# Kernel optimization log

Measured on AMD Instinct MI355X. Metric: run time of the kernel, lower is better.

## Reference

```python
import jax, jax.numpy as jnp
import numpy as np

N_FFT = 2048
HOP = 441
DIM = 512


def _hann(n_fft):
    # torch.hann_window (periodic): 0.5*(1 - cos(2*pi*n/N))
    n = jnp.arange(n_fft, dtype=jnp.float32)
    return 0.5 * (1.0 - jnp.cos(2.0 * jnp.pi * n / n_fft))


def setup_inputs() -> dict:
    key = jax.random.key(0)
    k1, k2, k3 = jax.random.split(key, 3)
    x = jax.random.normal(k1, (4, 2, 1323000), dtype=jnp.float32)
    W_enc = 1e-4 * jax.random.normal(k2, (DIM, N_FFT), dtype=jnp.float32)
    W_dec = 1e-4 * jax.random.normal(k3, (N_FFT, DIM), dtype=jnp.float32)
    return {"x": x, "W_enc": W_enc, "W_dec": W_dec, "length": 1323000}


def reference(x, W_enc, W_dec, length):
    b, c, L = x.shape
    pad = N_FFT // 2
    window = _hann(N_FFT)

    # ---- encode ----
    xp = jnp.pad(x, ((0, 0), (0, 0), (pad, pad)), mode="reflect")  # (b,c,L+n_fft)
    Lp = xp.shape[-1]
    t = (Lp - N_FFT) // HOP + 1  # num frames
    idx = jnp.arange(t)[:, None] * HOP + jnp.arange(N_FFT)[None, :]  # (t, n)
    frames = xp[..., idx] * window  # (b,c,t,n) -- the overlapping unfold buffer
    feat = jnp.einsum("bctn,mn->bctm", frames, W_enc)  # (b,c,t,dim)

    # ---- decode ----
    rec = jnp.einsum("bctm,nm->bctn", feat, W_dec)  # (b,c,t,n)
    L2 = N_FFT + (t - 1) * HOP
    # overlap-add (F.fold) over merged (b*c) rows
    out = jnp.zeros((b * c, L2), dtype=rec.dtype)
    out = out.at[:, idx].add(rec.reshape(b * c, t, N_FFT))
    # window normalization (second fold in the original)
    win_norm = jnp.zeros((L2,), dtype=rec.dtype)
    win_norm = win_norm.at[idx].add(jnp.broadcast_to(window, (t, N_FFT)))
    out = out / jnp.clip(win_norm, 1e-8)
    out = out.reshape(b, c, L2)[..., pad:pad + length]
    return out
```

## Files before the change

### kernel.cpp

```cpp
#include <hip/hip_runtime.h>
#include <stdint.h>

typedef unsigned short u16;
typedef unsigned int u32;
typedef __attribute__((ext_vector_type(8))) short short8;
typedef __attribute__((ext_vector_type(4))) float f32x4;

#define L_IN   1323000
#define PAD    1024
#define HOP    441
#define T_FR   3001
#define M_ROWS 24008
#define NB     3008
#define RPAD   448
#define K1E    2240
#define K2     2560
#define W_2PI_N 3.0679615757712823e-3f

__device__ __forceinline__ u16 f2bf(float f) {
  union { float f; u32 u; } v; v.f = f;
  u32 r = v.u + 0x7FFFu + ((v.u >> 16) & 1u);
  return (u16)(r >> 16);
}

__device__ __forceinline__ void gload16(const void* g, void* l) {
  __builtin_amdgcn_global_load_lds(
      (const __attribute__((address_space(1))) u32*)g,
      (__attribute__((address_space(3))) u32*)l, 16, 0, 0);
}

__global__ void prep_all(const float* __restrict__ x,
                         const float* __restrict__ W_enc, const float* __restrict__ W_dec,
                         u16* __restrict__ xb, u16* __restrict__ wh2,
                         u16* __restrict__ b2, float* __restrict__ zeros) {
  int stride = gridDim.x * blockDim.x;
  int tid0 = blockIdx.x * blockDim.x + threadIdx.x;
  for (int idx = tid0; idx < 64; idx += stride) zeros[idx] = 0.f;
  for (int idx = tid0; idx < 8 * NB * RPAD; idx += stride) {
    int bc = idx / (NB * RPAD);
    int rem = idx - bc * (NB * RPAD);
    int u = rem / RPAD;
    int r = rem - u * RPAD;
    int s = HOP * u + r - PAD;
    int ja = s < 0 ? -s : s;
    int jb = 2 * L_IN - 2 - ja;
    int jr = ja < jb ? ja : jb;
    xb[idx] = f2bf(x[(size_t)bc * L_IN + jr]);
  }
  for (int idx = tid0; idx < 512 * K1E; idx += stride) {
    int m = idx / K1E;
    int k = idx - m * K1E;
    int j = k / RPAD;
    int r = k - j * RPAD;
    int n = HOP * j + r;
    float v = 0.f;
    if (r < HOP && n < 2048)
      v = (0.5f - 0.5f * cosf(W_2PI_N * (float)n)) * W_enc[m * 2048 + n];
    wh2[idx] = f2bf(v);
  }
  for (int idx = tid0; idx < 512 * K2; idx += stride) {
    int r = idx / K2;
    int k = idx - r * K2;
    int j = k >> 9;
    int m = k & 511;
    int n = HOP * j + r;
    float v = (r < HOP && n < 2048) ? W_dec[n * 512 + m] : 0.f;
    b2[idx] = f2bf(v);
  }
}

__device__ __forceinline__ void mfma_tile(const u16* sA, const u16* sB, f32x4 acc[4][4],
                                          int lane, int wr, int wc) {
  const int lr = lane & 15;
  const int hi = lane >> 4;
  #pragma unroll
  for (int ks = 0; ks < 2; ++ks) {
    const int off = (((ks * 4 + hi) ^ (lr & 7)) << 3);
    short8 af[4], bg[4];
    #pragma unroll
    for (int f = 0; f < 4; ++f)
      af[f] = *(const short8*)(sA + (wr + f * 16 + lr) * 64 + off);
    #pragma unroll
    for (int f = 0; f < 4; ++f)
      bg[f] = *(const short8*)(sB + (wc + f * 16 + lr) * 64 + off);
    #pragma unroll
    for (int mf = 0; mf < 4; ++mf)
      #pragma unroll
      for (int nf = 0; nf < 4; ++nf)
        acc[mf][nf] = __builtin_amdgcn_mfma_f32_16x16x32_bf16(af[mf], bg[nf], acc[mf][nf], 0, 0, 0);
  }
}


__global__ __launch_bounds__(256, 2)
void gemm_enc(const u16* __restrict__ xb, const u16* __restrict__ wh2,
              u16* __restrict__ featb) {
  __shared__ u16 sA[128 * 64];
  __shared__ u16 sB[128 * 64];
  const int tid = threadIdx.x;
  const int lane = tid & 63;
  const int w = tid >> 6;
  const int m0 = blockIdx.x * 128;
  const int n0 = blockIdx.y * 128;
  const int colsw = (((lane & 7) ^ ((lane >> 3) & 7)) << 3);

  const u16* bsrc[4];
  const u16* asrc[4];
  #pragma unroll
  for (int i = 0; i < 4; ++i) {
    int row = (i * 4 + w) * 8 + (lane >> 3);
    bsrc[i] = wh2 + (size_t)(n0 + row) * K1E + colsw;
    int rg = m0 + row;
    int rgc = rg < M_ROWS ? rg : (M_ROWS - 1);
    int bc = rgc / T_FR;
    int t  = rgc - bc * T_FR;
    asrc[i] = xb + ((size_t)bc * NB + t) * RPAD + colsw;
  }

  f32x4 acc[4][4];
  #pragma unroll
  for (int a = 0; a < 4; ++a)
    #pragma unroll
    for (int b = 0; b < 4; ++b) acc[a][b] = f32x4{0.f, 0.f, 0.f, 0.f};

  const int wr = (w >> 1) * 64, wc = (w & 1) * 64;

  for (int kc = 0; kc < K1E; kc += 64) {
    __syncthreads();
    #pragma unroll
    for (int i = 0; i < 4; ++i)
      gload16(bsrc[i] + kc, &sB[(i * 4 + w) * 512]);
    #pragma unroll
    for (int i = 0; i < 4; ++i)
      gload16(asrc[i] + kc, &sA[(i * 4 + w) * 512]);
    __syncthreads();
    mfma_tile(sA, sB, acc, lane, wr, wc);
  }

  #pragma unroll
  for (int mf = 0; mf < 4; ++mf) {
    #pragma unroll
    for (int e = 0; e < 4; ++e) {
      int rg = m0 + wr + mf * 16 + ((lane >> 4) << 2) + e;
      if (rg < M_ROWS) {
        #pragma unroll
        for (int nf = 0; nf < 4; ++nf) {
          int cg = n0 + wc + nf * 16 + (lane & 15);
          featb[(size_t)rg * 512 + cg] = f2bf(acc[mf][nf][e]);
        }
      }
    }
  }
}


__global__ __launch_bounds__(256, 2)
void gemm_dec(const u16* __restrict__ featb, const u16* __restrict__ b2,
              const u16* __restrict__ zeros, float* __restrict__ out) {
  __shared__ u16 sA[128 * 64];
  __shared__ u16 sB[128 * 64];
  const int tid = threadIdx.x;
  const int lane = tid & 63;
  const int w = tid >> 6;
  const int m0 = blockIdx.x * 128;
  const int n0 = blockIdx.y * 128;
  const int colsw = (((lane & 7) ^ ((lane >> 3) & 7)) << 3);

  const u16* bsrc[4];
  const u16* fsrc[4];
  int qiv[4];
  unsigned vmask = 0;
  #pragma unroll
  for (int i = 0; i < 4; ++i) {
    int row = (i * 4 + w) * 8 + (lane >> 3);
    bsrc[i] = b2 + (size_t)(n0 + row) * K2 + colsw;
    int rg = m0 + row;
    int rgc = rg < M_ROWS ? rg : (M_ROWS - 1);
    int bc = rgc / T_FR;
    int qi = rgc - bc * T_FR;
    if (rg < M_ROWS) vmask |= 1u << i;
    qiv[i] = qi;
    fsrc[i] = featb + (size_t)(bc * T_FR + qi + 2) * 512 + colsw;
  }

  f32x4 acc[4][4];
  #pragma unroll
  for (int a = 0; a < 4; ++a)
    #pragma unroll
    for (int b = 0; b < 4; ++b) acc[a][b] = f32x4{0.f, 0.f, 0.f, 0.f};

  const int wr = (w >> 1) * 64, wc = (w & 1) * 64;

  for (int kc = 0; kc < K2; kc += 64) {
    int j = kc >> 9;
    __syncthreads();
    #pragma unroll
    for (int i = 0; i < 4; ++i)
      gload16(bsrc[i] + kc, &sB[(i * 4 + w) * 512]);
    #pragma unroll
    for (int i = 0; i < 4; ++i) {
      int t = qiv[i] + 2 - j;
      bool ok = ((vmask >> i) & 1) && (t >= 0) && (t <= 3000);
      const u16* pa = ok ? (fsrc[i] + kc - 1024 * j) : (zeros + colsw);
      gload16(pa, &sA[(i * 4 + w) * 512]);
    }
    __syncthreads();
    mfma_tile(sA, sB, acc, lane, wr, wc);
  }

  const int lr16 = lane & 15;
  float hh[4][5];
  float rnfull[4];
  int cgv[4];
  #pragma unroll
  for (int nf = 0; nf < 4; ++nf) {
    int cg = n0 + wc + nf * 16 + lr16;
    cgv[nf] = cg;
    float s = 0.f;
    #pragma unroll
    for (int j = 0; j < 5; ++j) {
      int n = HOP * j + cg;
      float h = (cg < HOP && n < 2048) ? (0.5f - 0.5f * cosf(W_2PI_N * (float)n)) : 0.f;
      hh[nf][j] = h;
      s += h;
    }
    rnfull[nf] = 1.f / fmaxf(s, 1e-8f);
  }

  #pragma unroll
  for (int mf = 0; mf < 4; ++mf) {
    #pragma unroll
    for (int e = 0; e < 4; ++e) {
      int rg = m0 + wr + mf * 16 + ((lane >> 4) << 2) + e;
      if (rg < M_ROWS) {
        int bc = rg / T_FR;
        int qi = rg - bc * T_FR;
        int ib = HOP * qi - 142;
        bool interior = (qi >= 2) && (qi <= 2998);
        #pragma unroll
        for (int nf = 0; nf < 4; ++nf) {
          if (cgv[nf] < HOP) {
            int oi = ib + cgv[nf];
            if (oi >= 0 && oi < L_IN) {
              float rn;
              if (interior) {
                rn = rnfull[nf];
              } else {
                float s = 0.f;
                #pragma unroll
                for (int j = 0; j < 5; ++j)
                  if ((unsigned)(qi + 2 - j) <= 3000u) s += hh[nf][j];
                rn = 1.f / fmaxf(s, 1e-8f);
              }
              out[(size_t)bc * L_IN + oi] = acc[mf][nf][e] * rn;
            }
          }
        }
      }
    }
  }
}


extern "C" void kernel_launch(void* const* d_in, const int* in_sizes, int n_in,
                              void* d_out, int out_size, void* d_ws, size_t ws_size,
                              hipStream_t stream) {
  const float* x     = (const float*)d_in[0];
  const float* W_enc = (const float*)d_in[1];
  const float* W_dec = (const float*)d_in[2];
  float* out = (float*)d_out;
  char* ws = (char*)d_ws;

  u16* xb = (u16*)d_out;

  u16*   wh2   = (u16*)  (ws + 0);
  u16*   b2    = (u16*)  (ws + 2293760);
  u16*   featb = (u16*)  (ws + 4915200);
  float* zeros = (float*)(ws + 29499392);

  prep_all<<<2048, 256, 0, stream>>>(x, W_enc, W_dec, xb, wh2, b2, zeros);
  gemm_enc<<<dim3(188, 4), 256, 0, stream>>>(xb, wh2, featb);
  gemm_dec<<<dim3(188, 4), 256, 0, stream>>>(featb, b2, (const u16*)zeros, out);
}
```

Before: 152.7 us.

## Double-buffer LDS tiles in both GEMMs to overlap global loads with MFMA

Both the encoder and decoder GEMMs now use two LDS buffers for the A and B tiles. The next K-chunk is prefetched asynchronously with global_load_lds while MFMAs run on the current one, using a vmcnt wait and raw barriers instead of two __syncthreads per iteration. Wave priority is raised during the MFMA section. The aim is to hide global-memory latency, at the cost of doubling LDS per block (64KB), which may limit occupancy to two blocks per CU.

```diff
diff --git a/kernel.cpp b/kernel.cpp
--- a/kernel.cpp
+++ b/kernel.cpp
@@ -95,8 +95,10 @@
 __global__ __launch_bounds__(256, 2)
 void gemm_enc(const u16* __restrict__ xb, const u16* __restrict__ wh2,
               u16* __restrict__ featb) {
-  __shared__ u16 sA[128 * 64];
-  __shared__ u16 sB[128 * 64];
+  __shared__ u16 sA0[128 * 64];
+  __shared__ u16 sB0[128 * 64];
+  __shared__ u16 sA1[128 * 64];
+  __shared__ u16 sB1[128 * 64];
   const int tid = threadIdx.x;
   const int lane = tid & 63;
   const int w = tid >> 6;
@@ -124,17 +126,34 @@
     for (int b = 0; b < 4; ++b) acc[a][b] = f32x4{0.f, 0.f, 0.f, 0.f};
 
   const int wr = (w >> 1) * 64, wc = (w & 1) * 64;
-
-  for (int kc = 0; kc < K1E; kc += 64) {
-    __syncthreads();
+  const int ldoff = w * 512;
+
+  auto stage = [&](int kc, u16* dA, u16* dB) {
     #pragma unroll
     for (int i = 0; i < 4; ++i)
-      gload16(bsrc[i] + kc, &sB[(i * 4 + w) * 512]);
+      gload16(bsrc[i] + kc, dB + i * 2048 + ldoff);
     #pragma unroll
     for (int i = 0; i < 4; ++i)
-      gload16(asrc[i] + kc, &sA[(i * 4 + w) * 512]);
-    __syncthreads();
-    mfma_tile(sA, sB, acc, lane, wr, wc);
+      gload16(asrc[i] + kc, dA + i * 2048 + ldoff);
+  };
+
+  const int NT = K1E / 64;
+  stage(0, sA0, sB0);
+  #pragma unroll 1
+  for (int it = 0; it < NT; ++it) {
+    u16* cA = (it & 1) ? sA1 : sA0;
+    u16* cB = (it & 1) ? sB1 : sB0;
+    if (it + 1 < NT) {
+      stage((it + 1) * 64, (it & 1) ? sA0 : sA1, (it & 1) ? sB0 : sB1);
+      asm volatile("s_waitcnt vmcnt(8)" ::: "memory");
+    } else {
+      asm volatile("s_waitcnt vmcnt(0)" ::: "memory");
+    }
+    __builtin_amdgcn_s_barrier();
+    __builtin_amdgcn_s_setprio(1);
+    mfma_tile(cA, cB, acc, lane, wr, wc);
+    __builtin_amdgcn_s_setprio(0);
+    __builtin_amdgcn_s_barrier();
   }
 
   #pragma unroll
@@ -157,8 +176,10 @@
 __global__ __launch_bounds__(256, 2)
 void gemm_dec(const u16* __restrict__ featb, const u16* __restrict__ b2,
               const u16* __restrict__ zeros, float* __restrict__ out) {
-  __shared__ u16 sA[128 * 64];
-  __shared__ u16 sB[128 * 64];
+  __shared__ u16 sA0[128 * 64];
+  __shared__ u16 sB0[128 * 64];
+  __shared__ u16 sA1[128 * 64];
+  __shared__ u16 sB1[128 * 64];
   const int tid = threadIdx.x;
   const int lane = tid & 63;
   const int w = tid >> 6;
@@ -190,22 +211,39 @@
     for (int b = 0; b < 4; ++b) acc[a][b] = f32x4{0.f, 0.f, 0.f, 0.f};
 
   const int wr = (w >> 1) * 64, wc = (w & 1) * 64;
-
-  for (int kc = 0; kc < K2; kc += 64) {
+  const int ldoff = w * 512;
+
+  auto stage = [&](int kc, u16* dA, u16* dB) {
     int j = kc >> 9;
-    __syncthreads();
     #pragma unroll
     for (int i = 0; i < 4; ++i)
-      gload16(bsrc[i] + kc, &sB[(i * 4 + w) * 512]);
+      gload16(bsrc[i] + kc, dB + i * 2048 + ldoff);
     #pragma unroll
     for (int i = 0; i < 4; ++i) {
       int t = qiv[i] + 2 - j;
       bool ok = ((vmask >> i) & 1) && (t >= 0) && (t <= 3000);
       const u16* pa = ok ? (fsrc[i] + kc - 1024 * j) : (zeros + colsw);
-      gload16(pa, &sA[(i * 4 + w) * 512]);
-    }
-    __syncthreads();
-    mfma_tile(sA, sB, acc, lane, wr, wc);
+      gload16(pa, dA + i * 2048 + ldoff);
+    }
+  };
+
+  const int NT = K2 / 64;
+  stage(0, sA0, sB0);
+  #pragma unroll 1
+  for (int it = 0; it < NT; ++it) {
+    u16* cA = (it & 1) ? sA1 : sA0;
+    u16* cB = (it & 1) ? sB1 : sB0;
+    if (it + 1 < NT) {
+      stage((it + 1) * 64, (it & 1) ? sA0 : sA1, (it & 1) ? sB0 : sB1);
+      asm volatile("s_waitcnt vmcnt(8)" ::: "memory");
+    } else {
+      asm volatile("s_waitcnt vmcnt(0)" ::: "memory");
+    }
+    __builtin_amdgcn_s_barrier();
+    __builtin_amdgcn_s_setprio(1);
+    mfma_tile(cA, cB, acc, lane, wr, wc);
+    __builtin_amdgcn_s_setprio(0);
+    __builtin_amdgcn_s_barrier();
   }
 
   const int lr16 = lane & 15;
```

Measured after the change: 206.5 us. 35.3% more time.
